# Kernel optimization log

Measured on AMD Instinct MI355X. Metric: run time of the kernel, lower is better.

The kernel has to match this reference:

```python
import jax, jax.numpy as jnp
import numpy as np

# --- problem constants (match init_kwargs / input_specs) ---
FS = 50.0            # sampling rate (Hz)
WINDOW_FREQ = 0.5    # running-abs-mean window (Hz); >0 -> RAM whitening branch
F1, F2 = 0.1, 10.0   # taper corner frequencies (Hz)
NCH, NPTS = 1000, 30000
XCOR = 2 * NPTS - 1          # 59999
FAST = 65536                 # nextpow2(XCOR)


def setup_inputs() -> dict:
    key = jax.random.key(0)
    k1, k2 = jax.random.split(key)
    return {
        "data1": jax.random.normal(k1, (NCH, NPTS), dtype=jnp.float32),
        "data2": jax.random.normal(k2, (NCH, NPTS), dtype=jnp.float32),
    }


def _running_abs_mean_whiten(rfft, nwin):
    """Vectorized equivalent of per-channel running_absolute_mean:
    pad |spec| by nwin edge values each side, box-filter (scipy 'same'
    alignment => window tmp[i+off+1 : i+off+1+nwin], off=(nwin-1)//2),
    then divide spectrum by the smoothed magnitude."""
    nch, nf = rfft.shape
    off = (nwin - 1) // 2
    a = jnp.abs(rfft)  # [nch, nf]
    tmp = jnp.concatenate(
        [jnp.broadcast_to(a[:, :1], (nch, nwin)), a,
         jnp.broadcast_to(a[:, -1:], (nch, nwin))], axis=1)  # [nch, nf+2*nwin]
    cs = jnp.pad(jnp.cumsum(tmp, axis=1), ((0, 0), (1, 0)))   # leading zero
    smoothed = (cs[:, off + 1 + nwin: off + 1 + nwin + nf]
                - cs[:, off + 1: off + 1 + nf]) / nwin
    return jnp.nan_to_num(rfft / smoothed)


def _spectral_whitening(rfft, df):
    nf = rfft.shape[-1]
    idxf1 = int(np.floor(F1 / df))
    idxf2 = int(np.ceil(F2 / df))
    nwin = int(WINDOW_FREQ / df)
    w = _running_abs_mean_whiten(rfft, nwin)
    # cosine-squared tapers outside [f1, f2]
    taper_lo = jnp.cos(jnp.linspace(np.pi / 2, np.pi, idxf1)) ** 2
    taper_hi = jnp.cos(jnp.linspace(np.pi, np.pi / 2, nf - idxf2)) ** 2
    w = w.at[:, :idxf1].multiply(taper_lo)
    w = w.at[:, idxf2:].multiply(taper_hi)
    return w


def reference(data1, data2):
    df = FS / FAST
    f1 = jnp.fft.rfft(data1, n=FAST, axis=-1)
    f2 = jnp.fft.rfft(data2, n=FAST, axis=-1)
    f1 = _spectral_whitening(f1, df)
    f2 = _spectral_whitening(f2, df)
    cc = jnp.fft.irfft(jnp.conj(f1) * f2, n=FAST, axis=-1)  # [nch, FAST]
    cc = jnp.roll(cc, FAST // 2, axis=-1)
    start = FAST // 2 - XCOR // 2
    return cc[:, start:start + XCOR]  # [nch, 2*npts-1]
```

## Files before the change

kernel.cpp:

```cpp
#include <hip/hip_runtime.h>

#define PI_F 3.14159265358979323846f

#define NCH   1000
#define NPTS  30000
#define NHALF 15000
#define NFFT  32768
#define NBF32 1024
#define STR   32770
#define XCOR  59999

#define UC 0.99518472667219693f
#define US 0.09801714032956060f

__device__ __forceinline__ float2 cadd(float2 a, float2 b){ return make_float2(a.x+b.x, a.y+b.y); }
__device__ __forceinline__ float2 csub(float2 a, float2 b){ return make_float2(a.x-b.x, a.y-b.y); }
__device__ __forceinline__ float2 cmul(float2 a, float2 b){ return make_float2(a.x*b.x - a.y*b.y, a.x*b.y + a.y*b.x); }

template<int S>
__device__ __forceinline__ float2 mulIs(float2 z){ return make_float2(-(float)S*z.y, (float)S*z.x); }

template<int S>
__device__ __forceinline__ void dft8(float2 v[8]){
  const float r2 = 0.7071067811865476f;
  const float sf = (float)S;
  float2 ea=cadd(v[0],v[4]), eb=csub(v[0],v[4]);
  float2 ec=cadd(v[2],v[6]), ed=csub(v[2],v[6]);
  float2 oa=cadd(v[1],v[5]), ob=csub(v[1],v[5]);
  float2 oc=cadd(v[3],v[7]), od=csub(v[3],v[7]);
  float2 ied=mulIs<S>(ed), iod=mulIs<S>(od);
  float2 E0=cadd(ea,ec), E2=csub(ea,ec), E1=cadd(eb,ied), E3=csub(eb,ied);
  float2 O0=cadd(oa,oc), O2=csub(oa,oc), O1=cadd(ob,iod), O3=csub(ob,iod);
  float2 T1 = make_float2(r2*(O1.x - sf*O1.y), r2*(O1.y + sf*O1.x));
  float2 T2 = mulIs<S>(O2);
  float2 T3 = make_float2(r2*(-O3.x - sf*O3.y), r2*(sf*O3.x - O3.y));
  v[0]=cadd(E0,O0); v[4]=csub(E0,O0);
  v[1]=cadd(E1,T1); v[5]=csub(E1,T1);
  v[2]=cadd(E2,T2); v[6]=csub(E2,T2);
  v[3]=cadd(E3,T3); v[7]=csub(E3,T3);
}

template<int S>
__device__ __forceinline__ void dft4(float2 v[4]){
  float2 t0=cadd(v[0],v[2]), t1=csub(v[0],v[2]);
  float2 t2=cadd(v[1],v[3]), t3=mulIs<S>(csub(v[1],v[3]));
  v[0]=cadd(t0,t2); v[2]=csub(t0,t2);
  v[1]=cadd(t1,t3); v[3]=csub(t1,t3);
}

template<int S>
__device__ __forceinline__ void dft32(float2 v[32]){
  constexpr float TC[22] = {
    1.f, 0.98078528040323044f, 0.92387953251128674f, 0.83146961230254524f,
    0.70710678118654757f, 0.55557023301960218f, 0.38268343236508978f, 0.19509032201612825f,
    0.f, -0.19509032201612825f, -0.38268343236508978f, -0.55557023301960218f,
    -0.70710678118654757f, -0.83146961230254524f, -0.92387953251128674f, -0.98078528040323044f,
    -1.f, -0.98078528040323044f, -0.92387953251128674f, -0.83146961230254524f,
    -0.70710678118654757f, -0.55557023301960218f };
  constexpr float TS[22] = {
    0.f, 0.19509032201612825f, 0.38268343236508978f, 0.55557023301960218f,
    0.70710678118654757f, 0.83146961230254524f, 0.92387953251128674f, 0.98078528040323044f,
    1.f, 0.98078528040323044f, 0.92387953251128674f, 0.83146961230254524f,
    0.70710678118654757f, 0.55557023301960218f, 0.38268343236508978f, 0.19509032201612825f,
    0.f, -0.19509032201612825f, -0.38268343236508978f, -0.55557023301960218f,
    -0.70710678118654757f, -0.83146961230254524f };
  float2 y[4][8];
  #pragma unroll
  for (int b = 0; b < 4; ++b)
    #pragma unroll
    for (int a = 0; a < 8; ++a) y[b][a] = v[4*a + b];
  #pragma unroll
  for (int b = 0; b < 4; ++b) dft8<S>(y[b]);
  #pragma unroll
  for (int b = 1; b < 4; ++b)
    #pragma unroll
    for (int k1 = 1; k1 < 8; ++k1) {
      int m = b*k1;
      float2 w = make_float2(TC[m], (float)S * TS[m]);
      y[b][k1] = cmul(y[b][k1], w);
    }
  #pragma unroll
  for (int k1 = 0; k1 < 8; ++k1) {
    float2 z[4] = { y[0][k1], y[1][k1], y[2][k1], y[3][k1] };
    dft4<S>(z);
    #pragma unroll
    for (int k2 = 0; k2 < 4; ++k2) v[k1 + 8*k2] = z[k2];
  }
}

template<int S>
__device__ __forceinline__ void stage_twiddle32(float2 v[32], float ang){
  float s1,c1,s8,c8;
  __sincosf(ang, &s1, &c1);
  __sincosf(8.f*ang, &s8, &c8);
  float2 w1 = make_float2(c1, s1), w8 = make_float2(c8, s8);
  float2 w16 = cmul(w8, w8), w24 = cmul(w16, w8);
  float2 base[4] = { make_float2(1.f, 0.f), w8, w16, w24 };
  #pragma unroll
  for (int m = 0; m < 4; ++m) {
    float2 wr = base[m];
    if (m > 0) v[8*m] = cmul(v[8*m], wr);
    #pragma unroll
    for (int l = 1; l < 8; ++l) { wr = cmul(wr, w1); v[8*m+l] = cmul(v[8*m+l], wr); }
  }
}

__global__ __launch_bounds__(256) void fft_fwd_fused(const float* __restrict__ d1, const float* __restrict__ d2,
                                                     float2* __restrict__ out, int cb, int ch0)
{
  __shared__ float2 lds[256*33];
  const int bid = blockIdx.x;
  const int c = bid >> 2, b = bid & 3;
  const int t = threadIdx.x;
  const float* src = (c < cb) ? (d1 + (size_t)(ch0 + c) * NPTS)
                              : (d2 + (size_t)(ch0 + c - cb) * NPTS);
  const float2* src2 = reinterpret_cast<const float2*>(src);

  const int j1 = 8*b + (t & 7) + 32*(t >> 3);
  float2 v[32];
  #pragma unroll
  for (int r = 0; r < 32; ++r) {
    int m = j1 + (r << 10);
    v[r] = (m < NHALF) ? src2[m] : make_float2(0.f, 0.f);
  }
  dft32<-1>(v);
  #pragma unroll
  for (int r = 0; r < 32; ++r) lds[t*33 + r] = v[r];
  __syncthreads();

  const int d = t >> 5, jm = t & 31;
  #pragma unroll
  for (int r = 0; r < 32; ++r) v[r] = lds[(d + 8*r)*33 + jm];
  stage_twiddle32<-1>(v, -(2.0f*PI_F) * (float)jm * (1.0f/1024.0f));
  dft32<-1>(v);
  const int j2 = 256*b + t;
  float2* dst = out + (size_t)c * STR + ((j2 >> 5) << 10) + jm;
  #pragma unroll
  for (int r = 0; r < 32; ++r) dst[(size_t)(r << 5)] = v[r];
}

template<int LG, int S>
__global__ __launch_bounds__(256) void fft_pass32(const float2* __restrict__ in, float2* __restrict__ out)
{
  int tid = blockIdx.x*256 + threadIdx.x;
  int c = tid >> 10;
  int j = tid & (NBF32-1);
  const float2* src = in + (size_t)c * STR;
  float2 v[32];
  #pragma unroll
  for (int r = 0; r < 32; ++r) v[r] = src[j + (r << 10)];
  constexpr int NS = 1 << LG;
  int jm = j & (NS - 1);
  if constexpr (LG > 0) {
    float ang = (float)S * (2.0f*PI_F) * (float)jm / (float)(NS*32);
    stage_twiddle32<S>(v, ang);
  }
  dft32<S>(v);
  int idxD = ((j >> LG) << (LG+5)) + jm;
  float2* dst = out + (size_t)c * STR + idxD;
  #pragma unroll
  for (int r = 0; r < 32; ++r) dst[(size_t)(r << LG)] = v[r];
}

__device__ __forceinline__ int padidx(int m){ return m + (m >> 5); }

__global__ __launch_bounds__(1024) void whiten_kernel(float2* __restrict__ buf)
{
  const int ch = blockIdx.x;
  const int t  = threadIdx.x;
  float2* Z = buf + (size_t)ch * STR;
  __shared__ float s[33793];
  __shared__ float wsums[16];

  float2 X[33];
  #pragma unroll
  for (int i = 0; i < 33; ++i) {
    int k = i*1024 + t;
    if (i < 32 || t == 0) {
      float2 zk = Z[k & (NFFT-1)];
      float2 zn = Z[(NFFT - k) & (NFFT-1)];
      float2 xe = make_float2(0.5f*(zk.x+zn.x), 0.5f*(zk.y-zn.y));
      float2 xh = make_float2(0.5f*(zk.x-zn.x), 0.5f*(zk.y+zn.y));
      float2 xo = make_float2(xh.y, -xh.x);
      float ang = -PI_F * (float)k * (1.0f/32768.0f);
      float sn, cs; __sincosf(ang, &sn, &cs);
      float2 w = make_float2(cs, sn);
      X[i] = cadd(xe, cmul(w, xo));
      s[padidx(k)] = sqrtf(X[i].x*X[i].x + X[i].y*X[i].y);
    }
  }
  __syncthreads();

  const int base = t*32;
  float sum = 0.f;
  #pragma unroll
  for (int q = 0; q < 32; ++q) sum += s[padidx(base+q)];
  if (t == 1023) sum += s[padidx(32768)];
  const int lane = t & 63, wid = t >> 6;
  float v = sum;
  #pragma unroll
  for (int off = 1; off < 64; off <<= 1) {
    float u = __shfl_up(v, off);
    if (lane >= off) v += u;
  }
  if (lane == 63) wsums[wid] = v;
  __syncthreads();
  float wexcl = 0.f;
  for (int w = 0; w < 16; ++w) wexcl += (w < wid) ? wsums[w] : 0.f;
  float run = wexcl + (v - sum);
  #pragma unroll
  for (int q = 0; q < 32; ++q) {
    int idx = padidx(base+q);
    run += s[idx];
    s[idx] = run;
  }
  if (t == 1023) { int idx = padidx(32768); run += s[idx]; s[idx] = run; }
  __syncthreads();

  const float a0 = s[padidx(0)];
  const float alast = s[padidx(32768)] - s[padidx(32767)];
  #pragma unroll
  for (int i = 0; i < 33; ++i) {
    int k = i*1024 + t;
    if (i < 32 || t == 0) {
      int hi = k + 327; if (hi > 32768) hi = 32768;
      int lom1 = k - 328;
      float Shi = s[padidx(hi)];
      float Slo = (lom1 >= 0) ? s[padidx(lom1)] : 0.f;
      float lc = (k < 327) ? (float)(327 - k) : 0.f;
      float rc = (k > 32441) ? (float)(k - 32441) : 0.f;
      float smoothed = (lc*a0 + (Shi - Slo) + rc*alast) * (1.0f/655.0f);
      float2 wv;
      if (smoothed > 0.f) {
        float inv = 1.0f / smoothed;
        wv = make_float2(X[i].x*inv, X[i].y*inv);
      } else wv = make_float2(0.f, 0.f);
      float tp = 1.0f;
      if (k < 131)        { float th = (float)k * (PI_F/260.0f);           float sn = __sinf(th); tp = sn*sn; }
      else if (k >= 13108){ float th = (float)(k-13108) * (PI_F/39320.0f); float cs = __cosf(th); tp = cs*cs; }
      wv.x *= tp; wv.y *= tp;
      Z[k] = wv;
    }
  }
}

__global__ __launch_bounds__(256) void cross_inv0(const float2* __restrict__ W,
                                                  float2* __restrict__ out0, int cb)
{
  int tid = blockIdx.x*256 + threadIdx.x;
  int c = tid >> 10;
  int j = tid & 1023;
  const float2* W1 = W + (size_t)c * STR;
  const float2* W2 = W + (size_t)(cb + c) * STR;
  const float scale = 1.0f/32768.0f;
  float sj, cj; __sincosf(PI_F*(float)j*(1.0f/32768.0f), &sj, &cj);
  float2 pw = make_float2(cj, sj);
  const float2 pstep = make_float2(UC, US);
  float2 v[32];
  #pragma unroll
  for (int r = 0; r < 32; ++r) {
    int m = j + (r << 10);
    int mm = 32768 - m;
    float2 A  = W1[m],  B  = W2[m];
    float2 Am = W1[mm], Bm = W2[mm];
    float2 Ck = make_float2(A.x*B.x + A.y*B.y,     A.x*B.y - A.y*B.x);
    float2 Cn = make_float2(Am.x*Bm.x + Am.y*Bm.y, Am.x*Bm.y - Am.y*Bm.x);
    float2 xe = make_float2(0.5f*(Ck.x+Cn.x), 0.5f*(Ck.y-Cn.y));
    float2 d  = make_float2(0.5f*(Ck.x-Cn.x), 0.5f*(Ck.y+Cn.y));
    float2 xo = cmul(pw, d);
    v[r] = make_float2((xe.x - xo.y)*scale, (xe.y + xo.x)*scale);
    pw = cmul(pw, pstep);
  }
  dft32<1>(v);
  float4* o4 = reinterpret_cast<float4*>(out0 + (size_t)c * STR + (size_t)j * 32);
  #pragma unroll
  for (int r = 0; r < 32; r += 2)
    o4[r>>1] = make_float4(v[r].x, v[r].y, v[r+1].x, v[r+1].y);
}

__global__ __launch_bounds__(256) void fft_inv_final32(const float2* __restrict__ in, float* __restrict__ out, int ch0)
{
  int tid = blockIdx.x*256 + threadIdx.x;
  int c = tid >> 10;
  int j = tid & (NBF32-1);
  const float2* src = in + (size_t)c * STR;
  float2 v[32];
  #pragma unroll
  for (int r = 0; r < 32; ++r) v[r] = src[j + (r << 10)];
  float ang = (2.0f*PI_F) * (float)j * (1.0f/32768.0f);
  stage_twiddle32<1>(v, ang);
  dft32<1>(v);
  float* o = out + (size_t)(ch0 + c) * XCOR;
  #pragma unroll
  for (int r = 0; r < 32; ++r) {
    int n = j + (r << 10);
    int m = 2*n;
    int j1 = (m <= 29999) ? (m + 29999) : ((m >= 35537) ? (m - 35537) : -1);
    if (j1 >= 0) o[j1] = v[r].x;
    int m2 = m + 1;
    int j2 = (m2 <= 29999) ? (m2 + 29999) : ((m2 >= 35537) ? (m2 - 35537) : -1);
    if (j2 >= 0) o[j2] = v[r].y;
  }
}

__global__ void diag_kernel(float* out, float vv){ if (threadIdx.x==0 && blockIdx.x==0) out[0] = vv; }

extern "C" void kernel_launch(void* const* d_in, const int* in_sizes, int n_in,
                              void* d_out, int out_size, void* d_ws, size_t ws_size,
                              hipStream_t stream)
{
  const float* d1 = (const float*)d_in[0];
  const float* d2 = (const float*)d_in[1];
  float* out = (float*)d_out;

  const size_t bytesPerCh = 2ULL * 2ULL * (size_t)STR * sizeof(float2);
  int CB = (int)(ws_size / bytesPerCh);
  if (CB > NCH) CB = NCH;
  if (CB < 1) { diag_kernel<<<1,1,0,stream>>>(out, (float)ws_size); return; }

  float2* bufA = (float2*)d_ws;
  float2* bufB = bufA + (size_t)2 * CB * STR;

  for (int ch0 = 0; ch0 < NCH; ch0 += CB) {
    int cb = (NCH - ch0 < CB) ? (NCH - ch0) : CB;
    int nch2 = 2*cb;
    dim3 thr(256);

    fft_fwd_fused     <<<dim3(nch2*4), thr, 0, stream>>>(d1, d2, bufA, cb, ch0);
    fft_pass32<10,-1> <<<dim3(nch2*4), thr, 0, stream>>>(bufA, bufB);

    whiten_kernel     <<<dim3(nch2), dim3(1024), 0, stream>>>(bufB);

    cross_inv0        <<<dim3(cb*4), thr, 0, stream>>>(bufB, bufA, cb);

    fft_pass32<5,1>   <<<dim3(cb*4), thr, 0, stream>>>(bufA, bufB);
    fft_inv_final32   <<<dim3(cb*4), thr, 0, stream>>>(bufB, out, ch0);
  }
}
```

Baseline: 1.197 ms.

## Pair symmetric bins in cross-spectrum kernel and fuse last two inverse FFT passes

The cross-spectrum/unpack kernel now handles bins k and N-k together in one thread, so each loaded pair of spectra feeds two outputs. That roughly halves global reads of the whitened spectra, at the cost of a large shared-memory staging buffer per block. The two final inverse-FFT passes are merged into one kernel that does the middle radix-32 pass through LDS. This removes one full round trip of the intermediate buffer to global memory, but each of the four blocks per channel recomputes all middle-stage butterflies, which quadruples that arithmetic.

```diff
diff --git a/kernel.cpp b/kernel.cpp
--- a/kernel.cpp
+++ b/kernel.cpp
@@ -16,6 +16,9 @@
 __device__ __forceinline__ float2 cadd(float2 a, float2 b){ return make_float2(a.x+b.x, a.y+b.y); }
 __device__ __forceinline__ float2 csub(float2 a, float2 b){ return make_float2(a.x-b.x, a.y-b.y); }
 __device__ __forceinline__ float2 cmul(float2 a, float2 b){ return make_float2(a.x*b.x - a.y*b.y, a.x*b.y + a.y*b.x); }
+__device__ __forceinline__ float2 conjmul(float2 a, float2 b){
+  return make_float2(a.x*b.x + a.y*b.y, a.x*b.y - a.y*b.x);
+}
 
 template<int S>
 __device__ __forceinline__ float2 mulIs(float2 z){ return make_float2(-(float)S*z.y, (float)S*z.x); }
@@ -244,62 +247,135 @@
   }
 }
 
-__global__ __launch_bounds__(256) void cross_inv0(const float2* __restrict__ W,
-                                                  float2* __restrict__ out0, int cb)
-{
-  int tid = blockIdx.x*256 + threadIdx.x;
-  int c = tid >> 10;
-  int j = tid & 1023;
+__device__ __forceinline__ float2 pack_zinv(float2 Ck, float2 Cm, float2 pw){
+  const float scale = 1.0f/32768.0f;
+  float2 xe = make_float2(0.5f*(Ck.x+Cm.x), 0.5f*(Ck.y-Cm.y));
+  float2 d  = make_float2(0.5f*(Ck.x-Cm.x), 0.5f*(Ck.y+Cm.y));
+  float2 xo = cmul(pw, d);
+  return make_float2((xe.x - xo.y)*scale, (xe.y + xo.x)*scale);
+}
+
+__global__ __launch_bounds__(256) void cross_inv0_pair(const float2* __restrict__ W,
+                                                       float2* __restrict__ out0, int cb)
+{
+  __shared__ float2 zbs[256*33];
+  const int bid = blockIdx.x;
+  const int c = bid >> 1;
+  const int t = threadIdx.x;
+  const int p = ((bid & 1) << 8) + t;
   const float2* W1 = W + (size_t)c * STR;
   const float2* W2 = W + (size_t)(cb + c) * STR;
   const float scale = 1.0f/32768.0f;
-  float sj, cj; __sincosf(PI_F*(float)j*(1.0f/32768.0f), &sj, &cj);
-  float2 pw = make_float2(cj, sj);
-  const float2 pstep = make_float2(UC, US);
+  float2 zA[32];
+  float2* zB = zbs + t*33;
+
+  if (p != 0) {
+    const int q = 1024 - p;
+    float sp, cp; __sincosf(PI_F*(float)p*(1.0f/32768.0f), &sp, &cp);
+    float2 pw = make_float2(cp, sp);
+    const float2 pstep = make_float2(UC, US);
+    #pragma unroll
+    for (int r = 0; r < 32; ++r) {
+      int m  = p + (r << 10);
+      int mm = q + ((31 - r) << 10);
+      float2 Ck = conjmul(W1[m],  W2[m]);
+      float2 Cm = conjmul(W1[mm], W2[mm]);
+      zA[r]    = pack_zinv(Ck, Cm, pw);
+      zB[31-r] = pack_zinv(Cm, Ck, make_float2(-pw.x, pw.y));
+      pw = cmul(pw, pstep);
+    }
+  } else {
+    {
+      float2 Ck = conjmul(W1[0], W2[0]);
+      float2 Cm = conjmul(W1[32768], W2[32768]);
+      zA[0] = pack_zinv(Ck, Cm, make_float2(1.f, 0.f));
+    }
+    #pragma unroll
+    for (int i = 1; i < 16; ++i) {
+      int k = i << 10, km = 32768 - k;
+      float2 Ck = conjmul(W1[k],  W2[k]);
+      float2 Cm = conjmul(W1[km], W2[km]);
+      float sp2, cp2; __sincosf(PI_F*(float)k*(1.0f/32768.0f), &sp2, &cp2);
+      zA[i]    = pack_zinv(Ck, Cm, make_float2(cp2, sp2));
+      zA[32-i] = pack_zinv(Cm, Ck, make_float2(-cp2, sp2));
+    }
+    {
+      float2 Ck = conjmul(W1[16384], W2[16384]);
+      zA[16] = make_float2(Ck.x*scale, -Ck.y*scale);
+    }
+    #pragma unroll
+    for (int i = 0; i < 16; ++i) {
+      int k = (i << 10) + 512, km = 32768 - k;
+      float2 Ck = conjmul(W1[k],  W2[k]);
+      float2 Cm = conjmul(W1[km], W2[km]);
+      float sp2, cp2; __sincosf(PI_F*(float)k*(1.0f/32768.0f), &sp2, &cp2);
+      zB[i]    = pack_zinv(Ck, Cm, make_float2(cp2, sp2));
+      zB[31-i] = pack_zinv(Cm, Ck, make_float2(-cp2, sp2));
+    }
+  }
+
+  dft32<1>(zA);
+  {
+    float4* o4 = reinterpret_cast<float4*>(out0 + (size_t)c*STR + (size_t)p*32);
+    #pragma unroll
+    for (int r = 0; r < 32; r += 2)
+      o4[r>>1] = make_float4(zA[r].x, zA[r].y, zA[r+1].x, zA[r+1].y);
+  }
+  {
+    float2 zq[32];
+    #pragma unroll
+    for (int r = 0; r < 32; ++r) zq[r] = zB[r];
+    dft32<1>(zq);
+    const int jout = (p == 0) ? 512 : (1024 - p);
+    float4* o4 = reinterpret_cast<float4*>(out0 + (size_t)c*STR + (size_t)jout*32);
+    #pragma unroll
+    for (int r = 0; r < 32; r += 2)
+      o4[r>>1] = make_float4(zq[r].x, zq[r].y, zq[r+1].x, zq[r+1].y);
+  }
+}
+
+__global__ __launch_bounds__(256) void fft_inv_fused(const float2* __restrict__ in,
+                                                     float* __restrict__ out, int ch0)
+{
+  __shared__ float2 lds[8*1024];
+  const int c = blockIdx.x;
+  const int b = blockIdx.y;
+  const int t = threadIdx.x;
+  const float2* src = in + (size_t)c * STR;
+
+  #pragma unroll 1
+  for (int u = 0; u < 4; ++u) {
+    const int j1 = t + (u << 8);
+    float2 v[32];
+    #pragma unroll
+    for (int r = 0; r < 32; ++r) v[r] = src[j1 + (r << 10)];
+    const int jm = j1 & 31;
+    stage_twiddle32<1>(v, (2.0f*PI_F) * (float)jm * (1.0f/1024.0f));
+    dft32<1>(v);
+    #pragma unroll
+    for (int s = 0; s < 8; ++s) lds[(s << 10) + j1] = v[8*b + s];
+  }
+  __syncthreads();
+
+  const int j2 = (b << 8) + t;
+  const int l = j2 & 31;
+  const int pg = (j2 >> 5) - (b << 3);
   float2 v[32];
   #pragma unroll
+  for (int r2 = 0; r2 < 32; ++r2) v[r2] = lds[(pg << 10) + l + (r2 << 5)];
+  stage_twiddle32<1>(v, (2.0f*PI_F) * (float)j2 * (1.0f/32768.0f));
+  dft32<1>(v);
+
+  float* o = out + (size_t)(ch0 + c) * XCOR;
+  #pragma unroll
   for (int r = 0; r < 32; ++r) {
-    int m = j + (r << 10);
-    int mm = 32768 - m;
-    float2 A  = W1[m],  B  = W2[m];
-    float2 Am = W1[mm], Bm = W2[mm];
-    float2 Ck = make_float2(A.x*B.x + A.y*B.y,     A.x*B.y - A.y*B.x);
-    float2 Cn = make_float2(Am.x*Bm.x + Am.y*Bm.y, Am.x*Bm.y - Am.y*Bm.x);
-    float2 xe = make_float2(0.5f*(Ck.x+Cn.x), 0.5f*(Ck.y-Cn.y));
-    float2 d  = make_float2(0.5f*(Ck.x-Cn.x), 0.5f*(Ck.y+Cn.y));
-    float2 xo = cmul(pw, d);
-    v[r] = make_float2((xe.x - xo.y)*scale, (xe.y + xo.x)*scale);
-    pw = cmul(pw, pstep);
-  }
-  dft32<1>(v);
-  float4* o4 = reinterpret_cast<float4*>(out0 + (size_t)c * STR + (size_t)j * 32);
-  #pragma unroll
-  for (int r = 0; r < 32; r += 2)
-    o4[r>>1] = make_float4(v[r].x, v[r].y, v[r+1].x, v[r+1].y);
-}
-
-__global__ __launch_bounds__(256) void fft_inv_final32(const float2* __restrict__ in, float* __restrict__ out, int ch0)
-{
-  int tid = blockIdx.x*256 + threadIdx.x;
-  int c = tid >> 10;
-  int j = tid & (NBF32-1);
-  const float2* src = in + (size_t)c * STR;
-  float2 v[32];
-  #pragma unroll
-  for (int r = 0; r < 32; ++r) v[r] = src[j + (r << 10)];
-  float ang = (2.0f*PI_F) * (float)j * (1.0f/32768.0f);
-  stage_twiddle32<1>(v, ang);
-  dft32<1>(v);
-  float* o = out + (size_t)(ch0 + c) * XCOR;
-  #pragma unroll
-  for (int r = 0; r < 32; ++r) {
-    int n = j + (r << 10);
+    int n = j2 + (r << 10);
     int m = 2*n;
-    int j1 = (m <= 29999) ? (m + 29999) : ((m >= 35537) ? (m - 35537) : -1);
-    if (j1 >= 0) o[j1] = v[r].x;
+    int j1o = (m <= 29999) ? (m + 29999) : ((m >= 35537) ? (m - 35537) : -1);
+    if (j1o >= 0) o[j1o] = v[r].x;
     int m2 = m + 1;
-    int j2 = (m2 <= 29999) ? (m2 + 29999) : ((m2 >= 35537) ? (m2 - 35537) : -1);
-    if (j2 >= 0) o[j2] = v[r].y;
+    int j2o = (m2 <= 29999) ? (m2 + 29999) : ((m2 >= 35537) ? (m2 - 35537) : -1);
+    if (j2o >= 0) o[j2o] = v[r].y;
   }
 }
 
@@ -331,9 +407,8 @@
 
     whiten_kernel     <<<dim3(nch2), dim3(1024), 0, stream>>>(bufB);
 
-    cross_inv0        <<<dim3(cb*4), thr, 0, stream>>>(bufB, bufA, cb);
-
-    fft_pass32<5,1>   <<<dim3(cb*4), thr, 0, stream>>>(bufA, bufB);
-    fft_inv_final32   <<<dim3(cb*4), thr, 0, stream>>>(bufB, out, ch0);
-  }
-}
+    cross_inv0_pair   <<<dim3(cb*2), thr, 0, stream>>>(bufB, bufA, cb);
+
+    fft_inv_fused     <<<dim3(cb, 4), thr, 0, stream>>>(bufA, out, ch0);
+  }
+}
```

After: 2.102 ms. 75.6% more time.

## Fuse last two inverse FFT passes via LDS and halve forward-pass shared memory

Applied to the files above, without the earlier changes.

Merges the inverse FFT pass32<5> and the final pass into one kernel that exchanges data through shared memory, removing a full global-memory round trip over the intermediate buffer and one kernel launch. The forward fused kernel and the new inverse kernel both move the transpose through a smaller LDS buffer in two halves. Only half the threads do the second-stage FFT in each half, which lowers LDS use and may raise occupancy but leaves threads idle and adds extra barriers.

```diff
diff --git a/kernel.cpp b/kernel.cpp
--- a/kernel.cpp
+++ b/kernel.cpp
@@ -105,10 +105,10 @@
   }
 }
 
-__global__ __launch_bounds__(256) void fft_fwd_fused(const float* __restrict__ d1, const float* __restrict__ d2,
-                                                     float2* __restrict__ out, int cb, int ch0)
-{
-  __shared__ float2 lds[256*33];
+__global__ __launch_bounds__(256) void fft_fwd_fused2(const float* __restrict__ d1, const float* __restrict__ d2,
+                                                      float2* __restrict__ out, int cb, int ch0)
+{
+  __shared__ float2 lds[16*264];
   const int bid = blockIdx.x;
   const int c = bid >> 2, b = bid & 3;
   const int t = threadIdx.x;
@@ -124,19 +124,37 @@
     v[r] = (m < NHALF) ? src2[m] : make_float2(0.f, 0.f);
   }
   dft32<-1>(v);
-  #pragma unroll
-  for (int r = 0; r < 32; ++r) lds[t*33 + r] = v[r];
-  __syncthreads();
-
-  const int d = t >> 5, jm = t & 31;
-  #pragma unroll
-  for (int r = 0; r < 32; ++r) v[r] = lds[(d + 8*r)*33 + jm];
-  stage_twiddle32<-1>(v, -(2.0f*PI_F) * (float)jm * (1.0f/1024.0f));
-  dft32<-1>(v);
-  const int j2 = 256*b + t;
-  float2* dst = out + (size_t)c * STR + ((j2 >> 5) << 10) + jm;
-  #pragma unroll
-  for (int r = 0; r < 32; ++r) dst[(size_t)(r << 5)] = v[r];
+
+  #pragma unroll
+  for (int rr = 0; rr < 16; ++rr) lds[rr*264 + t] = v[rr];
+  __syncthreads();
+  if (t < 128) {
+    const int d = t & 7, jm = t >> 3;
+    float2 w[32];
+    #pragma unroll
+    for (int r = 0; r < 32; ++r) w[r] = lds[jm*264 + d + 8*r];
+    stage_twiddle32<-1>(w, -(2.0f*PI_F) * (float)jm * (1.0f/1024.0f));
+    dft32<-1>(w);
+    float2* dst = out + (size_t)c * STR + ((size_t)(8*b + d) << 10) + jm;
+    #pragma unroll
+    for (int r = 0; r < 32; ++r) dst[(size_t)(r << 5)] = w[r];
+  }
+  __syncthreads();
+
+  #pragma unroll
+  for (int rr = 16; rr < 32; ++rr) lds[(rr-16)*264 + t] = v[rr];
+  __syncthreads();
+  if (t >= 128) {
+    const int d = t & 7, jm = t >> 3;
+    float2 w[32];
+    #pragma unroll
+    for (int r = 0; r < 32; ++r) w[r] = lds[(jm-16)*264 + d + 8*r];
+    stage_twiddle32<-1>(w, -(2.0f*PI_F) * (float)jm * (1.0f/1024.0f));
+    dft32<-1>(w);
+    float2* dst = out + (size_t)c * STR + ((size_t)(8*b + d) << 10) + jm;
+    #pragma unroll
+    for (int r = 0; r < 32; ++r) dst[(size_t)(r << 5)] = w[r];
+  }
 }
 
 template<int LG, int S>
@@ -278,28 +296,70 @@
     o4[r>>1] = make_float4(v[r].x, v[r].y, v[r+1].x, v[r+1].y);
 }
 
-__global__ __launch_bounds__(256) void fft_inv_final32(const float2* __restrict__ in, float* __restrict__ out, int ch0)
-{
-  int tid = blockIdx.x*256 + threadIdx.x;
-  int c = tid >> 10;
-  int j = tid & (NBF32-1);
+__global__ __launch_bounds__(256) void fft_inv_fused3(const float2* __restrict__ in,
+                                                      float* __restrict__ out, int ch0)
+{
+  __shared__ float2 lds[16*264];
+  const int c = blockIdx.x;
+  const int b = blockIdx.y;
+  const int t = threadIdx.x;
+  const int li = t & 7, s = t >> 3;
   const float2* src = in + (size_t)c * STR;
+
+  const int j1 = 8*b + li + 32*s;
   float2 v[32];
   #pragma unroll
-  for (int r = 0; r < 32; ++r) v[r] = src[j + (r << 10)];
-  float ang = (2.0f*PI_F) * (float)j * (1.0f/32768.0f);
-  stage_twiddle32<1>(v, ang);
+  for (int r = 0; r < 32; ++r) v[r] = src[j1 + (r << 10)];
+  stage_twiddle32<1>(v, (2.0f*PI_F) * (float)(8*b + li) * (1.0f/1024.0f));
   dft32<1>(v);
-  float* o = out + (size_t)(ch0 + c) * XCOR;
-  #pragma unroll
-  for (int r = 0; r < 32; ++r) {
-    int n = j + (r << 10);
-    int m = 2*n;
-    int j1 = (m <= 29999) ? (m + 29999) : ((m >= 35537) ? (m - 35537) : -1);
-    if (j1 >= 0) o[j1] = v[r].x;
-    int m2 = m + 1;
-    int j2 = (m2 <= 29999) ? (m2 + 29999) : ((m2 >= 35537) ? (m2 - 35537) : -1);
-    if (j2 >= 0) o[j2] = v[r].y;
+
+  #pragma unroll
+  for (int rr = 0; rr < 16; ++rr) lds[rr*264 + t] = v[rr];
+  __syncthreads();
+  if (t < 128) {
+    const int li2 = t & 7, q = t >> 3;
+    const int j2 = 8*b + li2 + 32*q;
+    float2 w[32];
+    #pragma unroll
+    for (int r2 = 0; r2 < 32; ++r2) w[r2] = lds[q*264 + li2 + 8*r2];
+    stage_twiddle32<1>(w, (2.0f*PI_F) * (float)j2 * (1.0f/32768.0f));
+    dft32<1>(w);
+    float* o = out + (size_t)(ch0 + c) * XCOR;
+    #pragma unroll
+    for (int r = 0; r < 32; ++r) {
+      int n = j2 + (r << 10);
+      int m = 2*n;
+      int j1o = (m <= 29999) ? (m + 29999) : ((m >= 35537) ? (m - 35537) : -1);
+      if (j1o >= 0) o[j1o] = w[r].x;
+      int m2 = m + 1;
+      int j2o = (m2 <= 29999) ? (m2 + 29999) : ((m2 >= 35537) ? (m2 - 35537) : -1);
+      if (j2o >= 0) o[j2o] = w[r].y;
+    }
+  }
+  __syncthreads();
+
+  #pragma unroll
+  for (int rr = 16; rr < 32; ++rr) lds[(rr-16)*264 + t] = v[rr];
+  __syncthreads();
+  if (t >= 128) {
+    const int li2 = t & 7, q = t >> 3;
+    const int j2 = 8*b + li2 + 32*q;
+    float2 w[32];
+    #pragma unroll
+    for (int r2 = 0; r2 < 32; ++r2) w[r2] = lds[(q-16)*264 + li2 + 8*r2];
+    stage_twiddle32<1>(w, (2.0f*PI_F) * (float)j2 * (1.0f/32768.0f));
+    dft32<1>(w);
+    float* o = out + (size_t)(ch0 + c) * XCOR;
+    #pragma unroll
+    for (int r = 0; r < 32; ++r) {
+      int n = j2 + (r << 10);
+      int m = 2*n;
+      int j1o = (m <= 29999) ? (m + 29999) : ((m >= 35537) ? (m - 35537) : -1);
+      if (j1o >= 0) o[j1o] = w[r].x;
+      int m2 = m + 1;
+      int j2o = (m2 <= 29999) ? (m2 + 29999) : ((m2 >= 35537) ? (m2 - 35537) : -1);
+      if (j2o >= 0) o[j2o] = w[r].y;
+    }
   }
 }
 
@@ -326,14 +386,13 @@
     int nch2 = 2*cb;
     dim3 thr(256);
 
-    fft_fwd_fused     <<<dim3(nch2*4), thr, 0, stream>>>(d1, d2, bufA, cb, ch0);
+    fft_fwd_fused2    <<<dim3(nch2*4), thr, 0, stream>>>(d1, d2, bufA, cb, ch0);
     fft_pass32<10,-1> <<<dim3(nch2*4), thr, 0, stream>>>(bufA, bufB);
 
     whiten_kernel     <<<dim3(nch2), dim3(1024), 0, stream>>>(bufB);
 
     cross_inv0        <<<dim3(cb*4), thr, 0, stream>>>(bufB, bufA, cb);
 
-    fft_pass32<5,1>   <<<dim3(cb*4), thr, 0, stream>>>(bufA, bufB);
-    fft_inv_final32   <<<dim3(cb*4), thr, 0, stream>>>(bufB, out, ch0);
-  }
-}
+    fft_inv_fused3    <<<dim3(cb, 4), thr, 0, stream>>>(bufA, out, ch0);
+  }
+}
```

Result: slower. 1.424 ms (+18.9%).
